# Optimization experiments

Hardware: AMD Instinct MI355X
Metric: run time of the kernel (lower is better)

## Reference

```python
import jax, jax.numpy as jnp
import numpy as np

N_LAYERS = 2
H = 16                      # num_heads
ARW = (1.0, 1.0)            # att_residual_weight
MCB = (0.0, 1.0)            # mask_clip_balancer
LN_EPS = 1e-5


def _ln(x, g, b):
    mu = jnp.mean(x, axis=-1, keepdims=True)
    var = jnp.mean(jnp.square(x - mu), axis=-1, keepdims=True)
    return (x - mu) * jax.lax.rsqrt(var + LN_EPS) * g + b


def _quick_gelu(u):
    return u * jax.nn.sigmoid(1.702 * u)


def setup_inputs() -> dict:
    key = jax.random.key(0)
    ks = jax.random.split(key, 8)
    L, B, C = 577, 8, 1024
    d_ff = 4 * C
    inp = {
        'x': jax.random.normal(ks[0], (L, B, C), jnp.float32),
        'att_bias': jax.random.normal(ks[1], (N_LAYERS, B * H, L, L), jnp.float32),
        'ln1_g': jnp.ones((N_LAYERS, C), jnp.float32),
        'ln1_b': jnp.zeros((N_LAYERS, C), jnp.float32),
        'in_w': 0.02 * jax.random.normal(ks[2], (N_LAYERS, 3 * C, C), jnp.float32),
        'in_b': jnp.zeros((N_LAYERS, 3 * C), jnp.float32),
        'out_w': 0.02 * jax.random.normal(ks[3], (N_LAYERS, C, C), jnp.float32),
        'out_b': jnp.zeros((N_LAYERS, C), jnp.float32),
        'ln2_g': jnp.ones((N_LAYERS, C), jnp.float32),
        'ln2_b': jnp.zeros((N_LAYERS, C), jnp.float32),
        'fc1_w': 0.02 * jax.random.normal(ks[4], (N_LAYERS, d_ff, C), jnp.float32),
        'fc1_b': jnp.zeros((N_LAYERS, d_ff), jnp.float32),
        'fc2_w': 0.02 * jax.random.normal(ks[5], (N_LAYERS, C, d_ff), jnp.float32),
        'fc2_b': jnp.zeros((N_LAYERS, C), jnp.float32),
    }
    return inp


def reference(x, att_bias, ln1_g, ln1_b, in_w, in_b, out_w, out_b,
              ln2_g, ln2_b, fc1_w, fc1_b, fc2_w, fc2_b):
    L, B, C = x.shape
    d = C // H
    scale = d ** -0.5  # custom_att_factor is None
    for i in range(N_LAYERS):
        # --- custom CSA attention ---
        h = _ln(x, ln1_g[i], ln1_b[i])                              # [L,B,C]
        qkv = jnp.einsum('lbc,fc->lbf', h, in_w[i]) + in_b[i]       # [L,B,3C]
        q, k, v = jnp.split(qkv, 3, axis=-1)
        to_heads = lambda t: t.reshape(L, B, H, d).transpose(1, 2, 0, 3)  # [B,H,L,d]
        q, k, v = to_heads(q), to_heads(k), to_heads(v)
        bias = att_bias[i].reshape(B, H, L, L)
        q_attn = bias + scale * jnp.einsum('bhld,bhmd->bhlm', q, q)
        k_attn = bias + scale * jnp.einsum('bhld,bhmd->bhlm', k, k)
        attn = jax.nn.softmax(q_attn, axis=-1) + jax.nn.softmax(k_attn, axis=-1)
        attn = attn * 0.5                                           # norm_att=True
        attn = jnp.mean(attn, axis=1, keepdims=True)                # avg_att=True -> [B,1,L,L]
        out = jnp.matmul(attn, v)                                   # broadcast over H -> [B,H,L,d]
        out = MCB[0] * v + MCB[1] * out
        out = out.transpose(2, 0, 1, 3).reshape(L, B, C)
        out = jnp.einsum('lbc,oc->lbo', out, out_w[i]) + out_b[i]
        x = ARW[0] * x + ARW[1] * out
        # --- MLP residual ---
        h2 = _ln(x, ln2_g[i], ln2_b[i])
        u = _quick_gelu(jnp.einsum('lbc,fc->lbf', h2, fc1_w[i]) + fc1_b[i])
        x = x + jnp.einsum('lbf,cf->lbc', u, fc2_w[i]) + fc2_b[i]
    return x
```

## Files before the change

### kernel.cpp

```cpp
#include <hip/hip_runtime.h>

typedef float f32x4 __attribute__((ext_vector_type(4)));
typedef __bf16 bf16x8 __attribute__((ext_vector_type(8)));

#define L_SEQ 577
#define BB 8
#define CC 1024
#define HH 16
#define ROWS (L_SEQ*BB)

static __device__ __forceinline__ ushort f2b(float f) {
  unsigned u = __float_as_uint(f);
  u += 0x7fffu + ((u >> 16) & 1u);
  return (ushort)(u >> 16);
}

static __device__ __forceinline__ void gld16(const void* g, void* l) {
  __builtin_amdgcn_global_load_lds((const __attribute__((address_space(1))) void*)g,
                                   (__attribute__((address_space(3))) void*)l, 16, 0, 0);
}

__global__ void cvt_kernel(const float* __restrict__ src, ushort* __restrict__ dst, int n4) {
  int i = blockIdx.x * blockDim.x + threadIdx.x;
  if (i < n4) {
    float4 v = *(const float4*)(src + (size_t)i * 4);
    ushort4 o;
    o.x = f2b(v.x); o.y = f2b(v.y); o.z = f2b(v.z); o.w = f2b(v.w);
    *(ushort4*)(dst + (size_t)i * 4) = o;
  }
}

__global__ __launch_bounds__(256)
void ln_kernel(const float* __restrict__ x, const float* __restrict__ g,
               const float* __restrict__ be, ushort* __restrict__ out)
{
  const int row = blockIdx.x;
  const int t = threadIdx.x;
  const float* xr = x + (size_t)row * CC;
  float4 v = *(const float4*)(xr + t * 4);
  float s  = v.x + v.y + v.z + v.w;
  float s2 = v.x*v.x + v.y*v.y + v.z*v.z + v.w*v.w;
  #pragma unroll
  for (int sd = 1; sd < 64; sd <<= 1) { s += __shfl_xor(s, sd, 64); s2 += __shfl_xor(s2, sd, 64); }
  __shared__ float ps[4], ps2[4];
  const int w = t >> 6;
  if ((t & 63) == 0) { ps[w] = s; ps2[w] = s2; }
  __syncthreads();
  s  = ps[0] + ps[1] + ps[2] + ps[3];
  s2 = ps2[0] + ps2[1] + ps2[2] + ps2[3];
  const float mean = s * (1.f / 1024.f);
  const float var  = s2 * (1.f / 1024.f) - mean * mean;
  const float rstd = rsqrtf(var + 1e-5f);
  float4 gv = *(const float4*)(g + t * 4);
  float4 bv = *(const float4*)(be + t * 4);
  ushort4 o;
  o.x = f2b((v.x - mean) * rstd * gv.x + bv.x);
  o.y = f2b((v.y - mean) * rstd * gv.y + bv.y);
  o.z = f2b((v.z - mean) * rstd * gv.z + bv.z);
  o.w = f2b((v.w - mean) * rstd * gv.w + bv.w);
  *(ushort4*)(out + (size_t)row * CC + t * 4) = o;
}

__global__ __launch_bounds__(256)
void vt_kernel(const ushort* __restrict__ qkv, ushort* __restrict__ vt)
{
  __shared__ ushort tile[32][33];
  const int lt = blockIdx.x * 32;
  const int nt = blockIdx.y * 32;
  const int b  = blockIdx.z;
  const int tx = threadIdx.x & 31;
  const int ty = threadIdx.x >> 5;
  #pragma unroll
  for (int p = 0; p < 4; ++p) {
    int l = lt + ty + p * 8;
    ushort v = 0;
    if (l < L_SEQ) v = qkv[((size_t)l * BB + b) * 3072 + 2048 + nt + tx];
    tile[ty + p * 8][tx] = v;
  }
  __syncthreads();
  #pragma unroll
  for (int p = 0; p < 4; ++p) {
    int n = nt + ty + p * 8;
    int l = lt + tx;
    vt[((size_t)b * 1024 + n) * 608 + l] = tile[tx][ty + p * 8];
  }
}

__global__ __launch_bounds__(256, 2)
void attn_kernel(const ushort* __restrict__ qkv,
                 const float* __restrict__ bias,
                 ushort* __restrict__ attn)
{
  __shared__ float S[2][16][600];
  const int t = threadIdx.x;
  const int lane = t & 63;
  const int w = t >> 6;
  const int rb = blockIdx.x;
  const int b  = blockIdx.y;
  const int r0 = rb * 16;
  float acc[37];
  #pragma unroll
  for (int k = 0; k < 37; ++k) acc[k] = 0.f;

  const int fr = lane & 15;
  const int kc = (lane >> 4) * 8;
  const int arow = min(r0 + fr, L_SEQ - 1);
  const size_t abase = ((size_t)arow * BB + b) * 3072;

  for (int h = 0; h < HH; ++h) {
    const int qoff = h * 64;
    const int koff = CC + h * 64;
    bf16x8 aq0 = *(const bf16x8*)(qkv + abase + qoff + kc);
    bf16x8 aq1 = *(const bf16x8*)(qkv + abase + qoff + 32 + kc);
    bf16x8 ak0 = *(const bf16x8*)(qkv + abase + koff + kc);
    bf16x8 ak1 = *(const bf16x8*)(qkv + abase + koff + 32 + kc);
    for (int nt = w; nt < 37; nt += 4) {
      const int col = nt * 16 + fr;
      const int ncl = min(col, L_SEQ - 1);
      const size_t brow = ((size_t)ncl * BB + b) * 3072;
      bf16x8 bq0 = *(const bf16x8*)(qkv + brow + qoff + kc);
      bf16x8 bq1 = *(const bf16x8*)(qkv + brow + qoff + 32 + kc);
      bf16x8 bk0 = *(const bf16x8*)(qkv + brow + koff + kc);
      bf16x8 bk1 = *(const bf16x8*)(qkv + brow + koff + 32 + kc);
      f32x4 dq = {0.f, 0.f, 0.f, 0.f};
      f32x4 dk = {0.f, 0.f, 0.f, 0.f};
      dq = __builtin_amdgcn_mfma_f32_16x16x32_bf16(aq0, bq0, dq, 0, 0, 0);
      dq = __builtin_amdgcn_mfma_f32_16x16x32_bf16(aq1, bq1, dq, 0, 0, 0);
      dk = __builtin_amdgcn_mfma_f32_16x16x32_bf16(ak0, bk0, dk, 0, 0, 0);
      dk = __builtin_amdgcn_mfma_f32_16x16x32_bf16(ak1, bk1, dk, 0, 0, 0);
      const bool cvalid = (col < L_SEQ);
      #pragma unroll
      for (int r = 0; r < 4; ++r) {
        int row = (lane >> 4) * 4 + r;
        int l = min(r0 + row, L_SEQ - 1);
        float bs = bias[(((size_t)(b * HH + h)) * L_SEQ + l) * L_SEQ + min(col, L_SEQ - 1)];
        S[0][row][col] = cvalid ? (bs + 0.125f * dq[r]) : -1e30f;
        S[1][row][col] = cvalid ? (bs + 0.125f * dk[r]) : -1e30f;
      }
    }
    __syncthreads();
    const int rr = t >> 4;
    const int j0 = t & 15;
    #pragma unroll
    for (int v = 0; v < 2; ++v) {
      float mx = -1e30f;
      #pragma unroll
      for (int k = 0; k < 37; ++k) mx = fmaxf(mx, S[v][rr][j0 + 16 * k]);
      #pragma unroll
      for (int sd = 1; sd < 16; sd <<= 1) mx = fmaxf(mx, __shfl_xor(mx, sd, 16));
      float e[37]; float sm = 0.f;
      #pragma unroll
      for (int k = 0; k < 37; ++k) { e[k] = __expf(S[v][rr][j0 + 16 * k] - mx); sm += e[k]; }
      #pragma unroll
      for (int sd = 1; sd < 16; sd <<= 1) sm += __shfl_xor(sm, sd, 16);
      float inv = 0.03125f / sm;
      #pragma unroll
      for (int k = 0; k < 37; ++k) acc[k] += e[k] * inv;
    }
    __syncthreads();
  }
  const int rr = t >> 4;
  const int j0 = t & 15;
  const int l = r0 + rr;
  if (l < L_SEQ) {
    ushort* dst = attn + (size_t)b * 608 * 608 + (size_t)l * 608;
    #pragma unroll
    for (int k = 0; k < 37; ++k) dst[j0 + 16 * k] = f2b(acc[k]);
  }
}

template<int EPI>
__global__ __launch_bounds__(256, 2)
void gemm_bt(const ushort* __restrict__ A, int lda, int Arows, long aStride,
             const ushort* __restrict__ B, int ldb, long bStride,
             int M, int N, int K,
             const float* __restrict__ bias,
             float* __restrict__ xio,
             ushort* __restrict__ outb, int ldo)
{
  __shared__ __align__(16) ushort As[128 * 32];
  __shared__ __align__(16) ushort Bs[128 * 32];
  const int t = threadIdx.x;
  const int lane = t & 63;
  const int w = t >> 6;
  const int bm = blockIdx.x, bn = blockIdx.y, bz = blockIdx.z;
  const ushort* Ab = A + (long)bz * aStride;
  const ushort* Bb = B + (long)bz * bStride;
  const int srow = t >> 2;
  const int sc = (t & 3) * 8;
  const int wr = (w >> 1) * 64;
  const int wc = (w & 1) * 64;
  const int am1 = Arows - 1;
  f32x4 acc[4][4] = {};

  const int r0a = bm * 128 + srow;
  const int r0b = bn * 128 + srow;
  for (int kt = 0; kt < K; kt += 32) {
    __syncthreads();
    gld16(Ab + (size_t)min(r0a, am1) * lda + kt + sc, (void*)(As + t * 8));
    gld16(Ab + (size_t)min(r0a + 64, am1) * lda + kt + sc, (void*)(As + 2048 + t * 8));
    gld16(Bb + (size_t)r0b * ldb + kt + sc, (void*)(Bs + t * 8));
    gld16(Bb + (size_t)(r0b + 64) * ldb + kt + sc, (void*)(Bs + 2048 + t * 8));
    asm volatile("s_waitcnt vmcnt(0)" ::: "memory");
    __syncthreads();
    bf16x8 av[4], bv[4];
    const int fr = lane & 15;
    const int kc = (lane >> 4) * 8;
    #pragma unroll
    for (int m = 0; m < 4; ++m) av[m] = *(const bf16x8*)(As + (wr + m * 16 + fr) * 32 + kc);
    #pragma unroll
    for (int n = 0; n < 4; ++n) bv[n] = *(const bf16x8*)(Bs + (wc + n * 16 + fr) * 32 + kc);
    #pragma unroll
    for (int m = 0; m < 4; ++m)
      #pragma unroll
      for (int n = 0; n < 4; ++n)
        acc[m][n] = __builtin_amdgcn_mfma_f32_16x16x32_bf16(av[m], bv[n], acc[m][n], 0, 0, 0);
  }
  const int rbase = wr + (lane >> 4) * 4;
  const int cbase = wc + (lane & 15);
  #pragma unroll
  for (int n = 0; n < 4; ++n) {
    const int gn = bn * 128 + cbase + n * 16;
    const float bval = (EPI == 3) ? 0.f : bias[gn];
    #pragma unroll
    for (int m = 0; m < 4; ++m) {
      f32x4 d = acc[m][n];
      #pragma unroll
      for (int r = 0; r < 4; ++r) {
        const int gm = bm * 128 + rbase + m * 16 + r;
        if (gm < M) {
          if (EPI == 0) {
            outb[(size_t)gm * ldo + gn] = f2b(d[r] + bval);
          } else if (EPI == 1) {
            float v0 = d[r] + bval;
            outb[(size_t)gm * ldo + gn] = f2b(v0 / (1.f + __expf(-1.702f * v0)));
          } else if (EPI == 2) {
            xio[(size_t)gm * ldo + gn] += d[r] + bval;
          } else {
            outb[((size_t)gm * 8 + bz) * ldo + gn] = f2b(d[r]);
          }
        }
      }
    }
  }
}

extern "C" void kernel_launch(void* const* d_in, const int* in_sizes, int n_in,
                              void* d_out, int out_size, void* d_ws, size_t ws_size,
                              hipStream_t stream)
{
  (void)in_sizes; (void)n_in; (void)out_size; (void)ws_size;
  const float* x_in  = (const float*)d_in[0];
  const float* attb  = (const float*)d_in[1];
  const float* ln1_g = (const float*)d_in[2];
  const float* ln1_b = (const float*)d_in[3];
  const float* in_w  = (const float*)d_in[4];
  const float* in_b  = (const float*)d_in[5];
  const float* out_w = (const float*)d_in[6];
  const float* out_b = (const float*)d_in[7];
  const float* ln2_g = (const float*)d_in[8];
  const float* ln2_b = (const float*)d_in[9];
  const float* fc1_w = (const float*)d_in[10];
  const float* fc1_b = (const float*)d_in[11];
  const float* fc2_w = (const float*)d_in[12];
  const float* fc2_b = (const float*)d_in[13];
  float* x = (float*)d_out;

  char* ws = (char*)d_ws;
  size_t off = 0;
  auto alloc = [&](size_t bytes) -> void* {
    void* p = ws + off; off += (bytes + 255) & ~(size_t)255; return p;
  };
  ushort* wIn   = (ushort*)alloc(2ull * 3072 * 1024 * 2);
  ushort* wOut  = (ushort*)alloc(2ull * 1024 * 1024 * 2);
  ushort* wF1   = (ushort*)alloc(2ull * 4096 * 1024 * 2);
  ushort* wF2   = (ushort*)alloc(2ull * 4096 * 1024 * 2);
  ushort* hbuf  = (ushort*)alloc((size_t)ROWS * 1024 * 2);
  ushort* qkv   = (ushort*)alloc((size_t)ROWS * 3072 * 2);
  ushort* vt    = (ushort*)alloc((size_t)8 * 1024 * 608 * 2);
  ushort* attn  = (ushort*)alloc((size_t)8 * 608 * 608 * 2);
  ushort* outlb = (ushort*)alloc((size_t)ROWS * 1024 * 2);
  ushort* ubuf  = qkv;

  cvt_kernel<<<2 * 3072 * 1024 / 4 / 256, 256, 0, stream>>>(in_w,  wIn,  2 * 3072 * 1024 / 4);
  cvt_kernel<<<2 * 1024 * 1024 / 4 / 256, 256, 0, stream>>>(out_w, wOut, 2 * 1024 * 1024 / 4);
  cvt_kernel<<<2 * 4096 * 1024 / 4 / 256, 256, 0, stream>>>(fc1_w, wF1,  2 * 4096 * 1024 / 4);
  cvt_kernel<<<2 * 4096 * 1024 / 4 / 256, 256, 0, stream>>>(fc2_w, wF2,  2 * 4096 * 1024 / 4);
  hipMemcpyAsync(x, x_in, (size_t)ROWS * 1024 * 4, hipMemcpyDeviceToDevice, stream);

  for (int i = 0; i < 2; ++i) {
    ln_kernel<<<ROWS, 256, 0, stream>>>(x, ln1_g + i * 1024, ln1_b + i * 1024, hbuf);
    gemm_bt<0><<<dim3(37, 24, 1), 256, 0, stream>>>(hbuf, 1024, ROWS, 0,
        wIn + (size_t)i * 3072 * 1024, 1024, 0,
        ROWS, 3072, 1024, in_b + i * 3072, nullptr, qkv, 3072);
    attn_kernel<<<dim3(37, 8, 1), 256, 0, stream>>>(qkv, attb + (size_t)i * 128 * 577 * 577, attn);
    vt_kernel<<<dim3(19, 32, 8), 256, 0, stream>>>(qkv, vt);
    gemm_bt<3><<<dim3(5, 8, 8), 256, 0, stream>>>(attn, 608, 577, (long)608 * 608,
        vt, 608, (long)1024 * 608,
        577, 1024, 608, nullptr, nullptr, outlb, 1024);
    gemm_bt<2><<<dim3(37, 8, 1), 256, 0, stream>>>(outlb, 1024, ROWS, 0,
        wOut + (size_t)i * 1024 * 1024, 1024, 0,
        ROWS, 1024, 1024, out_b + i * 1024, x, nullptr, 1024);
    ln_kernel<<<ROWS, 256, 0, stream>>>(x, ln2_g + i * 1024, ln2_b + i * 1024, hbuf);
    gemm_bt<1><<<dim3(37, 32, 1), 256, 0, stream>>>(hbuf, 1024, ROWS, 0,
        wF1 + (size_t)i * 4096 * 1024, 1024, 0,
        ROWS, 4096, 1024, fc1_b + i * 4096, nullptr, ubuf, 4096);
    gemm_bt<2><<<dim3(37, 8, 1), 256, 0, stream>>>(ubuf, 4096, ROWS, 0,
        wF2 + (size_t)i * 4096 * 1024, 4096, 0,
        ROWS, 1024, 4096, fc2_b + i * 1024, x, nullptr, 1024);
  }
}
```

Measured before the change: 1.133 ms.

## Split attention over head groups and split-K the residual GEMMs with atomics

The attention kernel is now launched across 4 head groups. Each block accumulates its partial probability average into a float buffer with atomicAdd, and a conversion kernel then turns that buffer into bf16. The out-projection and fc2 GEMMs use split-K (2 and 4 ways), and their residual epilogue now uses atomicAdd into x, with the bias added only by the first K slice. The goal is to fill more CUs in undersized grids (296 blocks before). The cost is a memset, an extra conversion pass, atomic traffic and a nondeterministic summation order.

Measured after the change: 1.146 ms. About the same (+1.1%).

```diff
diff --git a/kernel.cpp b/kernel.cpp
--- a/kernel.cpp
+++ b/kernel.cpp
@@ -89,14 +89,15 @@
 __global__ __launch_bounds__(256, 2)
 void attn_kernel(const ushort* __restrict__ qkv,
                  const float* __restrict__ bias,
-                 ushort* __restrict__ attn)
-{
-  __shared__ float S[2][16][600];
+                 float* __restrict__ attnf)
+{
+  __shared__ float S[2][16][612];
   const int t = threadIdx.x;
   const int lane = t & 63;
   const int w = t >> 6;
   const int rb = blockIdx.x;
   const int b  = blockIdx.y;
+  const int hg = blockIdx.z;
   const int r0 = rb * 16;
   float acc[37];
   #pragma unroll
@@ -107,7 +108,8 @@
   const int arow = min(r0 + fr, L_SEQ - 1);
   const size_t abase = ((size_t)arow * BB + b) * 3072;
 
-  for (int h = 0; h < HH; ++h) {
+  for (int hh = 0; hh < 4; ++hh) {
+    const int h = hg * 4 + hh;
     const int qoff = h * 64;
     const int koff = CC + h * 64;
     bf16x8 aq0 = *(const bf16x8*)(qkv + abase + qoff + kc);
@@ -163,9 +165,10 @@
   const int j0 = t & 15;
   const int l = r0 + rr;
   if (l < L_SEQ) {
-    ushort* dst = attn + (size_t)b * 608 * 608 + (size_t)l * 608;
-    #pragma unroll
-    for (int k = 0; k < 37; ++k) dst[j0 + 16 * k] = f2b(acc[k]);
+    float* dst = attnf + (size_t)b * 608 * 608 + (size_t)l * 608;
+    #pragma unroll
+    for (int k = 0; k < 37; ++k)
+      if (j0 + 16 * k < L_SEQ) atomicAdd(dst + j0 + 16 * k, acc[k]);
   }
 }
 
@@ -173,7 +176,7 @@
 __global__ __launch_bounds__(256, 2)
 void gemm_bt(const ushort* __restrict__ A, int lda, int Arows, long aStride,
              const ushort* __restrict__ B, int ldb, long bStride,
-             int M, int N, int K,
+             int M, int N, int K, int kSplit,
              const float* __restrict__ bias,
              float* __restrict__ xio,
              ushort* __restrict__ outb, int ldo)
@@ -184,8 +187,16 @@
   const int lane = t & 63;
   const int w = t >> 6;
   const int bm = blockIdx.x, bn = blockIdx.y, bz = blockIdx.z;
-  const ushort* Ab = A + (long)bz * aStride;
-  const ushort* Bb = B + (long)bz * bStride;
+  int k0 = 0, k1 = K;
+  const ushort* Ab = A;
+  const ushort* Bb = B;
+  if (kSplit > 1) {
+    const int kc0 = K / kSplit;
+    k0 = bz * kc0; k1 = k0 + kc0;
+  } else {
+    Ab += (long)bz * aStride;
+    Bb += (long)bz * bStride;
+  }
   const int srow = t >> 2;
   const int sc = (t & 3) * 8;
   const int wr = (w >> 1) * 64;
@@ -195,7 +206,7 @@
 
   const int r0a = bm * 128 + srow;
   const int r0b = bn * 128 + srow;
-  for (int kt = 0; kt < K; kt += 32) {
+  for (int kt = k0; kt < k1; kt += 32) {
     __syncthreads();
     gld16(Ab + (size_t)min(r0a, am1) * lda + kt + sc, (void*)(As + t * 8));
     gld16(Ab + (size_t)min(r0a + 64, am1) * lda + kt + sc, (void*)(As + 2048 + t * 8));
@@ -221,7 +232,7 @@
   #pragma unroll
   for (int n = 0; n < 4; ++n) {
     const int gn = bn * 128 + cbase + n * 16;
-    const float bval = (EPI == 3) ? 0.f : bias[gn];
+    const float bval = (EPI == 3) ? 0.f : ((k0 == 0) ? bias[gn] : 0.f);
     #pragma unroll
     for (int m = 0; m < 4; ++m) {
       f32x4 d = acc[m][n];
@@ -235,7 +246,7 @@
             float v0 = d[r] + bval;
             outb[(size_t)gm * ldo + gn] = f2b(v0 / (1.f + __expf(-1.702f * v0)));
           } else if (EPI == 2) {
-            xio[(size_t)gm * ldo + gn] += d[r] + bval;
+            atomicAdd(xio + (size_t)gm * ldo + gn, d[r] + bval);
           } else {
             outb[((size_t)gm * 8 + bz) * ldo + gn] = f2b(d[r]);
           }
@@ -279,6 +290,7 @@
   ushort* qkv   = (ushort*)alloc((size_t)ROWS * 3072 * 2);
   ushort* vt    = (ushort*)alloc((size_t)8 * 1024 * 608 * 2);
   ushort* attn  = (ushort*)alloc((size_t)8 * 608 * 608 * 2);
+  float*  attnf = (float*)alloc((size_t)8 * 608 * 608 * 4);
   ushort* outlb = (ushort*)alloc((size_t)ROWS * 1024 * 2);
   ushort* ubuf  = qkv;
 
@@ -292,21 +304,23 @@
     ln_kernel<<<ROWS, 256, 0, stream>>>(x, ln1_g + i * 1024, ln1_b + i * 1024, hbuf);
     gemm_bt<0><<<dim3(37, 24, 1), 256, 0, stream>>>(hbuf, 1024, ROWS, 0,
         wIn + (size_t)i * 3072 * 1024, 1024, 0,
-        ROWS, 3072, 1024, in_b + i * 3072, nullptr, qkv, 3072);
-    attn_kernel<<<dim3(37, 8, 1), 256, 0, stream>>>(qkv, attb + (size_t)i * 128 * 577 * 577, attn);
+        ROWS, 3072, 1024, 1, in_b + i * 3072, nullptr, qkv, 3072);
+    hipMemsetAsync(attnf, 0, (size_t)8 * 608 * 608 * 4, stream);
+    attn_kernel<<<dim3(37, 8, 4), 256, 0, stream>>>(qkv, attb + (size_t)i * 128 * 577 * 577, attnf);
     vt_kernel<<<dim3(19, 32, 8), 256, 0, stream>>>(qkv, vt);
+    cvt_kernel<<<8 * 608 * 608 / 4 / 256, 256, 0, stream>>>(attnf, attn, 8 * 608 * 608 / 4);
     gemm_bt<3><<<dim3(5, 8, 8), 256, 0, stream>>>(attn, 608, 577, (long)608 * 608,
         vt, 608, (long)1024 * 608,
-        577, 1024, 608, nullptr, nullptr, outlb, 1024);
-    gemm_bt<2><<<dim3(37, 8, 1), 256, 0, stream>>>(outlb, 1024, ROWS, 0,
+        577, 1024, 608, 1, nullptr, nullptr, outlb, 1024);
+    gemm_bt<2><<<dim3(37, 8, 2), 256, 0, stream>>>(outlb, 1024, ROWS, 0,
         wOut + (size_t)i * 1024 * 1024, 1024, 0,
-        ROWS, 1024, 1024, out_b + i * 1024, x, nullptr, 1024);
+        ROWS, 1024, 1024, 2, out_b + i * 1024, x, nullptr, 1024);
     ln_kernel<<<ROWS, 256, 0, stream>>>(x, ln2_g + i * 1024, ln2_b + i * 1024, hbuf);
     gemm_bt<1><<<dim3(37, 32, 1), 256, 0, stream>>>(hbuf, 1024, ROWS, 0,
         wF1 + (size_t)i * 4096 * 1024, 1024, 0,
-        ROWS, 4096, 1024, fc1_b + i * 4096, nullptr, ubuf, 4096);
-    gemm_bt<2><<<dim3(37, 8, 1), 256, 0, stream>>>(ubuf, 4096, ROWS, 0,
+        ROWS, 4096, 1024, 1, fc1_b + i * 4096, nullptr, ubuf, 4096);
+    gemm_bt<2><<<dim3(37, 8, 4), 256, 0, stream>>>(ubuf, 4096, ROWS, 0,
         wF2 + (size_t)i * 4096 * 1024, 4096, 0,
-        ROWS, 1024, 4096, fc2_b + i * 1024, x, nullptr, 1024);
-  }
-}
+        ROWS, 1024, 4096, 4, fc2_b + i * 1024, x, nullptr, 1024);
+  }
+}
```
